# Kernel optimization log

Measured on AMD Instinct MI355X. Metric: run time of the kernel, lower is better.

The kernel has to match this reference:

```python
import jax, jax.numpy as jnp
import numpy as np

DIM, DEPTH, HEADS, DIM_HEAD, MLP_DIM = 512, 6, 8, 64, 2048
INNER = HEADS * DIM_HEAD
EPS = 1e-5


def _layernorm(x, s, b):
    mu = jnp.mean(x, axis=-1, keepdims=True)
    var = jnp.mean(jnp.square(x - mu), axis=-1, keepdims=True)
    return (x - mu) * jax.lax.rsqrt(var + EPS) * s + b


def setup_inputs() -> dict:
    key = jax.random.key(0)
    ks = jax.random.split(key, 12)
    d = {
        "x": jax.random.normal(ks[0], (8, 1024, DIM), dtype=jnp.float32),
        "ln1_s": jnp.ones((DEPTH, DIM), jnp.float32),
        "ln1_b": jnp.zeros((DEPTH, DIM), jnp.float32),
        "w_qkv": jax.random.normal(ks[1], (DEPTH, DIM, 3 * INNER), dtype=jnp.float32) * (DIM ** -0.5),
        "w_out": jax.random.normal(ks[2], (DEPTH, INNER, DIM), dtype=jnp.float32) * (INNER ** -0.5),
        "b_out": jnp.zeros((DEPTH, DIM), jnp.float32),
        "ln2_s": jnp.ones((DEPTH, DIM), jnp.float32),
        "ln2_b": jnp.zeros((DEPTH, DIM), jnp.float32),
        "w1": jax.random.normal(ks[3], (DEPTH, DIM, MLP_DIM), dtype=jnp.float32) * (DIM ** -0.5),
        "b1": jnp.zeros((DEPTH, MLP_DIM), jnp.float32),
        "w2": jax.random.normal(ks[4], (DEPTH, MLP_DIM, DIM), dtype=jnp.float32) * (MLP_DIM ** -0.5),
        "b2": jnp.zeros((DEPTH, DIM), jnp.float32),
    }
    return d


def reference(x, ln1_s, ln1_b, w_qkv, w_out, b_out, ln2_s, ln2_b, w1, b1, w2, b2):
    b, n, _ = x.shape
    scale = DIM_HEAD ** -0.5
    for i in range(DEPTH):
        # --- PreNorm Attention with residual ---
        h = _layernorm(x, ln1_s[i], ln1_b[i])
        qkv = h @ w_qkv[i]                                  # [b, n, 3*inner]
        q, k, v = jnp.split(qkv, 3, axis=-1)
        q = q.reshape(b, n, HEADS, DIM_HEAD)
        k = k.reshape(b, n, HEADS, DIM_HEAD)
        v = v.reshape(b, n, HEADS, DIM_HEAD)
        dots = jnp.einsum('bihd,bjhd->bhij', q, k) * scale  # [b, h, n, n]
        attn = jax.nn.softmax(dots, axis=-1)
        out = jnp.einsum('bhij,bjhd->bihd', attn, v).reshape(b, n, INNER)
        x = out @ w_out[i] + b_out[i] + x
        # --- PreNorm FeedForward with residual ---
        h = _layernorm(x, ln2_s[i], ln2_b[i])
        h = jax.nn.gelu(h @ w1[i] + b1[i], approximate=False)
        x = h @ w2[i] + b2[i] + x
    return x
```

## Files before the change

kernel.cpp:

```cpp
#include <hip/hip_runtime.h>
#include <cstdint>
#include <cstddef>

#define M_TOK 8192
#define DIMM  512
#define HEADS 8
#define DH    64
#define MLPD  2048
#define DEPTH 6

typedef unsigned short u16;
typedef unsigned int   u32;
typedef __attribute__((ext_vector_type(8))) short short8;
typedef __attribute__((ext_vector_type(4))) float f32x4;

__device__ __forceinline__ float bf2f(u16 u){ return __uint_as_float(((u32)u) << 16); }
__device__ __forceinline__ u16 f2bf(float f){
    u32 x = __float_as_uint(f);
    u32 r = x + 0x7fffu + ((x >> 16) & 1u);
    return (u16)(r >> 16);
}
__device__ __forceinline__ u32 cvt_pk_bf16(float a, float b){
    u32 r;
    asm("v_cvt_pk_bf16_f32 %0, %1, %2" : "=v"(r) : "v"(a), "v"(b));
    return r;
}
__device__ __forceinline__ void async16(const u16* g, u16* l){
    __builtin_amdgcn_global_load_lds(
        (const __attribute__((address_space(1))) void*)(uintptr_t)(const void*)g,
        (__attribute__((address_space(3))) void*)(u32)(uintptr_t)(void*)l,
        16, 0, 0);
}

__global__ void k_transpose_cvt(const float* __restrict__ in, u16* __restrict__ out, int R, int C){
    __shared__ u16 tile[32][33];
    size_t zoff = (size_t)blockIdx.z * R * C;
    in += zoff; out += zoff;
    int c0 = blockIdx.x * 32, r0 = blockIdx.y * 32;
    int tx = threadIdx.x, ty = threadIdx.y;
    #pragma unroll
    for (int i = 0; i < 32; i += 8)
        tile[ty + i][tx] = f2bf(in[(size_t)(r0 + ty + i) * C + c0 + tx]);
    __syncthreads();
    #pragma unroll
    for (int i = 0; i < 32; i += 8)
        out[(size_t)(c0 + ty + i) * R + r0 + tx] = tile[tx][ty + i];
}

__global__ __launch_bounds__(256) void k_layernorm(const float* __restrict__ x,
                                                   const float* __restrict__ s,
                                                   const float* __restrict__ b,
                                                   u16* __restrict__ out){
    int row = blockIdx.x * 4 + (threadIdx.x >> 6);
    int lane = threadIdx.x & 63;
    const float* xp = x + (size_t)row * DIMM + lane * 8;
    float v[8];
    #pragma unroll
    for (int c = 0; c < 8; c++) v[c] = xp[c];
    float sum = 0.f, sq = 0.f;
    #pragma unroll
    for (int c = 0; c < 8; c++){ sum += v[c]; sq += v[c] * v[c]; }
    #pragma unroll
    for (int m = 32; m >= 1; m >>= 1){
        sum += __shfl_xor(sum, m);
        sq  += __shfl_xor(sq,  m);
    }
    float mu  = sum * (1.f / DIMM);
    float var = sq * (1.f / DIMM) - mu * mu;
    float rs  = rsqrtf(var + 1e-5f);
    u16* op = out + (size_t)row * DIMM + lane * 8;
    #pragma unroll
    for (int c = 0; c < 8; c++){
        int col = lane * 8 + c;
        op[c] = f2bf((v[c] - mu) * rs * s[col] + b[col]);
    }
}

__device__ __forceinline__ float gelu_exact(float v){
    return 0.5f * v * (1.f + erff(v * 0.70710678118654752f));
}

#define LDT64 72

template<int MODE>
__global__ __launch_bounds__(256) void k_gemm128b(const u16* __restrict__ A,
                                                  const u16* __restrict__ Bt,
                                                  const float* __restrict__ bias,
                                                  u16* __restrict__ Cout,
                                                  int M, int N, int K){
    __shared__ u16 As[128 * LDT64];
    __shared__ u16 Bs[128 * LDT64];
    int m0 = blockIdx.y * 128, n0 = blockIdx.x * 128;
    int t = threadIdx.x;
    int w = t >> 6, lane = t & 63;
    int mi = lane & 15, quad = lane >> 4;
    int wr = w >> 1, wc = w & 1;

    int grow = lane >> 3, gcol = (lane & 7) * 8;
    const u16* agl = A  + (size_t)(m0 + w * 32 + grow) * K + gcol;
    const u16* bgl = Bt + (size_t)(n0 + w * 32 + grow) * K + gcol;
    u16* asl = &As[(w * 32) * 64];
    u16* bsl = &Bs[(w * 32) * 64];

    f32x4 acc[4][4];
    #pragma unroll
    for (int mt = 0; mt < 4; mt++)
        #pragma unroll
        for (int nt = 0; nt < 4; nt++) acc[mt][nt] = (f32x4){0.f, 0.f, 0.f, 0.f};

    for (int k0 = 0; k0 < K; k0 += 64){
        __syncthreads();
        #pragma unroll
        for (int i = 0; i < 4; i++){
            async16(agl + (size_t)(i * 8) * K + k0, asl + i * 8 * 64);
            async16(bgl + (size_t)(i * 8) * K + k0, bsl + i * 8 * 64);
        }
        __syncthreads();
        #pragma unroll
        for (int kk = 0; kk < 64; kk += 32){
            short8 af[4], bf[4];
            #pragma unroll
            for (int mt = 0; mt < 4; mt++)
                af[mt] = *(const short8*)&As[(wr * 64 + mt * 16 + mi) * 64 + kk + quad * 8];
            #pragma unroll
            for (int nt = 0; nt < 4; nt++)
                bf[nt] = *(const short8*)&Bs[(wc * 64 + nt * 16 + mi) * 64 + kk + quad * 8];
            #pragma unroll
            for (int mt = 0; mt < 4; mt++)
                #pragma unroll
                for (int nt = 0; nt < 4; nt++)
                    acc[mt][nt] = __builtin_amdgcn_mfma_f32_16x16x32_bf16(af[mt], bf[nt], acc[mt][nt], 0, 0, 0);
        }
    }

    float bv[4];
    if (MODE == 1){
        #pragma unroll
        for (int nt = 0; nt < 4; nt++) bv[nt] = bias[n0 + wc * 64 + nt * 16 + mi];
    }
    __syncthreads();
    u16* cs = &As[w * 16 * LDT64];
    int erow = lane >> 2, ecol = (lane & 3) * 16;
    #pragma unroll
    for (int mt = 0; mt < 4; mt++){
        #pragma unroll
        for (int nt = 0; nt < 4; nt++)
            #pragma unroll
            for (int r = 0; r < 4; r++){
                float v = acc[mt][nt][r];
                if (MODE == 1) v = gelu_exact(v + bv[nt]);
                cs[(quad * 4 + r) * LDT64 + nt * 16 + mi] = f2bf(v);
            }
        uint4 c0 = *(const uint4*)&cs[erow * LDT64 + ecol];
        uint4 c1 = *(const uint4*)&cs[erow * LDT64 + ecol + 8];
        u16* cp = Cout + (size_t)(m0 + wr * 64 + mt * 16 + erow) * N + n0 + wc * 64 + ecol;
        *(uint4*)cp       = c0;
        *(uint4*)(cp + 8) = c1;
    }
}

__global__ __launch_bounds__(256) void k_gemm64_res(const u16* __restrict__ A,
                                                    const u16* __restrict__ Bt,
                                                    const float* __restrict__ bias,
                                                    float* __restrict__ xres,
                                                    int M, int N, int K){
    __shared__ u16 As[64 * LDT64];
    __shared__ u16 Bs[64 * LDT64];
    int m0 = blockIdx.y * 64, n0 = blockIdx.x * 64;
    int t = threadIdx.x;
    int w = t >> 6, lane = t & 63;
    int mi = lane & 15, quad = lane >> 4;

    int grow = lane >> 3, gcol = (lane & 7) * 8;
    const u16* agl = A  + (size_t)(m0 + w * 16 + grow) * K + gcol;
    const u16* bgl = Bt + (size_t)(n0 + w * 16 + grow) * K + gcol;
    u16* asl = &As[(w * 16) * 64];
    u16* bsl = &Bs[(w * 16) * 64];

    f32x4 acc[4];
    #pragma unroll
    for (int tt = 0; tt < 4; tt++) acc[tt] = (f32x4){0.f, 0.f, 0.f, 0.f};

    for (int k0 = 0; k0 < K; k0 += 64){
        __syncthreads();
        #pragma unroll
        for (int i = 0; i < 2; i++){
            async16(agl + (size_t)(i * 8) * K + k0, asl + i * 8 * 64);
            async16(bgl + (size_t)(i * 8) * K + k0, bsl + i * 8 * 64);
        }
        __syncthreads();
        short8 af0 = *(const short8*)&As[(w * 16 + mi) * 64 + quad * 8];
        short8 af1 = *(const short8*)&As[(w * 16 + mi) * 64 + quad * 8 + 32];
        #pragma unroll
        for (int tt = 0; tt < 4; tt++){
            short8 bf0 = *(const short8*)&Bs[(tt * 16 + mi) * 64 + quad * 8];
            short8 bf1 = *(const short8*)&Bs[(tt * 16 + mi) * 64 + quad * 8 + 32];
            acc[tt] = __builtin_amdgcn_mfma_f32_16x16x32_bf16(af0, bf0, acc[tt], 0, 0, 0);
            acc[tt] = __builtin_amdgcn_mfma_f32_16x16x32_bf16(af1, bf1, acc[tt], 0, 0, 0);
        }
    }

    float bv[4];
    #pragma unroll
    for (int tt = 0; tt < 4; tt++) bv[tt] = bias[n0 + tt * 16 + mi];
    __syncthreads();
    float* cs = (w < 2) ? ((float*)As + w * 16 * LDT64)
                        : ((float*)Bs + (w - 2) * 16 * LDT64);
    #pragma unroll
    for (int tt = 0; tt < 4; tt++)
        #pragma unroll
        for (int r = 0; r < 4; r++)
            cs[(quad * 4 + r) * LDT64 + tt * 16 + mi] = acc[tt][r] + bv[tt];
    int erow = lane >> 2, ecol = (lane & 3) * 16;
    float* xp = xres + (size_t)(m0 + w * 16 + erow) * N + n0 + ecol;
    #pragma unroll
    for (int j = 0; j < 4; j++){
        float4 cv = *(const float4*)&cs[erow * LDT64 + ecol + j * 4];
        float4 xv = *(const float4*)(xp + j * 4);
        xv.x += cv.x; xv.y += cv.y; xv.z += cv.z; xv.w += cv.w;
        *(float4*)(xp + j * 4) = xv;
    }
}

#define LDK 72
#define C1_LOG2E 0.18033688011112042f
#define C2_LOG2E 11.541560327111707f

__global__ __launch_bounds__(256) void k_flash(const u16* __restrict__ qkv, u16* __restrict__ out){
    __shared__ u16 Ks[64 * LDK];
    __shared__ u16 Vt[80 * LDK];
    __shared__ u16 Ps[4][32 * LDK];
    int wg = (blockIdx.x & 7) * 64 + (blockIdx.x >> 3);
    int qt = wg & 7, h = (wg >> 3) & 7, b = wg >> 6;
    int t = threadIdx.x;
    int w = t >> 6, lane = t & 63;
    int mi = lane & 15, quad = lane >> 4;

    for (int i = t; i < 16 * 64; i += 256){
        int d = i >> 6, kk = i & 63;
        Vt[(64 + d) * LDK + kk] = 0x3F80;
    }

    const u16* base = qkv + ((size_t)b * 1024) * 1536;
    int hoff = h * 64;

    short8 qf[2][2];
    #pragma unroll
    for (int qh = 0; qh < 2; qh++){
        int qrow = qt * 128 + w * 32 + qh * 16 + mi;
        const u16* qp = base + (size_t)qrow * 1536 + hoff + quad * 8;
        qf[qh][0] = *(const short8*)(qp);
        qf[qh][1] = *(const short8*)(qp + 32);
    }

    f32x4 o[2][4];
    f32x4 lacc[2];
    #pragma unroll
    for (int qh = 0; qh < 2; qh++){
        #pragma unroll
        for (int nb = 0; nb < 4; nb++) o[qh][nb] = (f32x4){0.f, 0.f, 0.f, 0.f};
        lacc[qh] = (f32x4){0.f, 0.f, 0.f, 0.f};
    }

    int kkey = t >> 2, kseg = t & 3;
    const u16* kgp = base + (size_t)kkey * 1536 + 512 + hoff + kseg * 16;
    int vkey = lane, vdg = w;
    const u16* vgp = base + (size_t)vkey * 1536 + 1024 + hoff + vdg * 16;

    for (int kt = 0; kt < 16; kt++){
        size_t koff = (size_t)kt * 64 * 1536;
        uint4 kv0 = *(const uint4*)(kgp + koff);
        uint4 kv1 = *(const uint4*)(kgp + koff + 8);
        uint4 vv0 = *(const uint4*)(vgp + koff);
        uint4 vv1 = *(const uint4*)(vgp + koff + 8);
        __syncthreads();
        *(uint4*)&Ks[kkey * LDK + kseg * 16]     = kv0;
        *(uint4*)&Ks[kkey * LDK + kseg * 16 + 8] = kv1;
        u16 vtmp[16];
        *(uint4*)&vtmp[0] = vv0;
        *(uint4*)&vtmp[8] = vv1;
        #pragma unroll
        for (int i = 0; i < 16; i++)
            Vt[(vdg * 16 + i) * LDK + vkey] = vtmp[i];
        __syncthreads();

        short8 kb[4][2];
        #pragma unroll
        for (int nb = 0; nb < 4; nb++){
            kb[nb][0] = *(const short8*)&Ks[(nb * 16 + mi) * LDK + quad * 8];
            kb[nb][1] = *(const short8*)&Ks[(nb * 16 + mi) * LDK + quad * 8 + 32];
        }
        #pragma unroll
        for (int qh = 0; qh < 2; qh++){
            #pragma unroll
            for (int nb = 0; nb < 4; nb++){
                f32x4 z = (f32x4){0.f, 0.f, 0.f, 0.f};
                z = __builtin_amdgcn_mfma_f32_16x16x32_bf16(qf[qh][0], kb[nb][0], z, 0, 0, 0);
                z = __builtin_amdgcn_mfma_f32_16x16x32_bf16(qf[qh][1], kb[nb][1], z, 0, 0, 0);
                float e0 = exp2f(fmaf(z[0], C1_LOG2E, -C2_LOG2E));
                float e1 = exp2f(fmaf(z[1], C1_LOG2E, -C2_LOG2E));
                float e2 = exp2f(fmaf(z[2], C1_LOG2E, -C2_LOG2E));
                float e3 = exp2f(fmaf(z[3], C1_LOG2E, -C2_LOG2E));
                u32 p01 = cvt_pk_bf16(e0, e1);
                u32 p23 = cvt_pk_bf16(e2, e3);
                u16* pp = &Ps[w][(qh * 16 + quad * 4) * LDK + nb * 16 + mi];
                pp[0]       = (u16)p01;
                pp[LDK]     = (u16)(p01 >> 16);
                pp[2 * LDK] = (u16)p23;
                pp[3 * LDK] = (u16)(p23 >> 16);
            }
        }
        short8 vb[4][2], lb[2];
        #pragma unroll
        for (int nb = 0; nb < 4; nb++){
            vb[nb][0] = *(const short8*)&Vt[(nb * 16 + mi) * LDK + quad * 8];
            vb[nb][1] = *(const short8*)&Vt[(nb * 16 + mi) * LDK + quad * 8 + 32];
        }
        lb[0] = *(const short8*)&Vt[(64 + mi) * LDK + quad * 8];
        lb[1] = *(const short8*)&Vt[(64 + mi) * LDK + quad * 8 + 32];
        #pragma unroll
        for (int qh = 0; qh < 2; qh++){
            const short8 a0 = *(const short8*)&Ps[w][(qh * 16 + mi) * LDK + quad * 8];
            const short8 a1 = *(const short8*)&Ps[w][(qh * 16 + mi) * LDK + quad * 8 + 32];
            #pragma unroll
            for (int nb = 0; nb < 4; nb++){
                o[qh][nb] = __builtin_amdgcn_mfma_f32_16x16x32_bf16(a0, vb[nb][0], o[qh][nb], 0, 0, 0);
                o[qh][nb] = __builtin_amdgcn_mfma_f32_16x16x32_bf16(a1, vb[nb][1], o[qh][nb], 0, 0, 0);
            }
            lacc[qh] = __builtin_amdgcn_mfma_f32_16x16x32_bf16(a0, lb[0], lacc[qh], 0, 0, 0);
            lacc[qh] = __builtin_amdgcn_mfma_f32_16x16x32_bf16(a1, lb[1], lacc[qh], 0, 0, 0);
        }
    }
    #pragma unroll
    for (int qh = 0; qh < 2; qh++){
        float invl[4];
        #pragma unroll
        for (int r = 0; r < 4; r++) invl[r] = 1.f / lacc[qh][r];
        u16* op = out + ((size_t)b * 1024 + qt * 128 + w * 32 + qh * 16) * 512 + hoff;
        #pragma unroll
        for (int nb = 0; nb < 4; nb++){
            u32 c01 = cvt_pk_bf16(o[qh][nb][0] * invl[0], o[qh][nb][1] * invl[1]);
            u32 c23 = cvt_pk_bf16(o[qh][nb][2] * invl[2], o[qh][nb][3] * invl[3]);
            u16* cp = op + (size_t)(quad * 4) * 512 + nb * 16 + mi;
            cp[0]       = (u16)c01;
            cp[512]     = (u16)(c01 >> 16);
            cp[2 * 512] = (u16)c23;
            cp[3 * 512] = (u16)(c23 >> 16);
        }
    }
}

extern "C" void kernel_launch(void* const* d_in, const int* in_sizes, int n_in,
                              void* d_out, int out_size, void* d_ws, size_t ws_size,
                              hipStream_t stream){
    const float* x_in  = (const float*)d_in[0];
    const float* ln1_s = (const float*)d_in[1];
    const float* ln1_b = (const float*)d_in[2];
    const float* w_qkv = (const float*)d_in[3];
    const float* w_out = (const float*)d_in[4];
    const float* b_out = (const float*)d_in[5];
    const float* ln2_s = (const float*)d_in[6];
    const float* ln2_b = (const float*)d_in[7];
    const float* w1    = (const float*)d_in[8];
    const float* b1    = (const float*)d_in[9];
    const float* w2    = (const float*)d_in[10];
    const float* b2    = (const float*)d_in[11];
    float* out = (float*)d_out;

    char* ws = (char*)d_ws;
    float* x_f32 = (float*)ws;   ws += (size_t)M_TOK * DIMM * 4;
    u16* bufA    = (u16*)ws;     ws += (size_t)M_TOK * DIMM * 2;
    u16* bufB    = (u16*)ws;     ws += (size_t)M_TOK * MLPD * 2;
    u16* wbase   = (u16*)ws;
    size_t per_layer_w = (size_t)(1536 + 512 + 2048 + 2048) * 512;

    size_t used_big = (size_t)(ws - (char*)d_ws) + per_layer_w * 2 * DEPTH;
    bool big = (ws_size >= used_big);

    u16* ln_out   = bufA;
    u16* attn_out = bufA;
    u16* qkv      = bufB;
    u16* mlp_h    = bufB;

    size_t x_bytes = (size_t)M_TOK * DIMM * sizeof(float);
    hipMemcpyAsync(x_f32, x_in, x_bytes, hipMemcpyDeviceToDevice, stream);

    const size_t off_qkv = 0;
    const size_t off_out = (size_t)1536 * 512;
    const size_t off_w1  = off_out + (size_t)512 * 512;
    const size_t off_w2  = off_w1 + (size_t)2048 * 512;

    if (big){
        k_transpose_cvt<<<dim3(48, 16, 6), dim3(32, 8), 0, stream>>>(w_qkv, wbase + off_qkv * DEPTH, 512, 1536);
        k_transpose_cvt<<<dim3(16, 16, 6), dim3(32, 8), 0, stream>>>(w_out, wbase + off_out * DEPTH, 512, 512);
        k_transpose_cvt<<<dim3(64, 16, 6), dim3(32, 8), 0, stream>>>(w1,    wbase + off_w1  * DEPTH, 512, 2048);
        k_transpose_cvt<<<dim3(16, 64, 6), dim3(32, 8), 0, stream>>>(w2,    wbase + off_w2  * DEPTH, 2048, 512);
    }

    for (int i = 0; i < DEPTH; i++){
        u16 *wqkvT, *woutT, *w1T, *w2T;
        if (big){
            wqkvT = wbase + off_qkv * DEPTH + (size_t)i * 1536 * 512;
            woutT = wbase + off_out * DEPTH + (size_t)i * 512 * 512;
            w1T   = wbase + off_w1  * DEPTH + (size_t)i * 2048 * 512;
            w2T   = wbase + off_w2  * DEPTH + (size_t)i * 512 * 2048;
        } else {
            wqkvT = wbase + off_qkv; woutT = wbase + off_out;
            w1T   = wbase + off_w1;  w2T   = wbase + off_w2;
            k_transpose_cvt<<<dim3(48, 16), dim3(32, 8), 0, stream>>>(w_qkv + (size_t)i * 512 * 1536, wqkvT, 512, 1536);
            k_transpose_cvt<<<dim3(16, 16), dim3(32, 8), 0, stream>>>(w_out + (size_t)i * 512 * 512,  woutT, 512, 512);
            k_transpose_cvt<<<dim3(64, 16), dim3(32, 8), 0, stream>>>(w1    + (size_t)i * 512 * 2048, w1T,   512, 2048);
            k_transpose_cvt<<<dim3(16, 64), dim3(32, 8), 0, stream>>>(w2    + (size_t)i * 2048 * 512, w2T,   2048, 512);
        }

        k_layernorm<<<dim3(M_TOK / 4), dim3(256), 0, stream>>>(x_f32, ln1_s + i * 512, ln1_b + i * 512, ln_out);
        k_gemm128b<0><<<dim3(12, 64), dim3(256), 0, stream>>>(ln_out, wqkvT, nullptr, qkv,
                                                              M_TOK, 1536, 512);
        k_flash<<<dim3(512), dim3(256), 0, stream>>>(qkv, attn_out);
        k_gemm64_res<<<dim3(8, 128), dim3(256), 0, stream>>>(attn_out, woutT, b_out + i * 512, x_f32,
                                                             M_TOK, 512, 512);
        k_layernorm<<<dim3(M_TOK / 4), dim3(256), 0, stream>>>(x_f32, ln2_s + i * 512, ln2_b + i * 512, ln_out);
        k_gemm128b<1><<<dim3(16, 64), dim3(256), 0, stream>>>(ln_out, w1T, b1 + i * 2048, mlp_h,
                                                              M_TOK, 2048, 512);
        k_gemm64_res<<<dim3(8, 128), dim3(256), 0, stream>>>(mlp_h, w2T, b2 + i * 512, x_f32,
                                                             M_TOK, 512, 2048);
    }
    hipMemcpyAsync(out, x_f32, x_bytes, hipMemcpyDeviceToDevice, stream);
}
```

Before: 1.332 ms.

## Double-buffer GEMM shared tiles and prefetch next K/V tile in attention

Both GEMM kernels now keep two shared-memory tile buffers and issue the async global-to-LDS loads for the next K slice while MFMAs run on the current one. This drops one barrier per iteration and hides global load latency. The attention kernel also loads the next K/V tile into registers right after the current tile is staged in LDS, so that load overlaps the QK and PV math. In exchange, LDS use per block doubles, which may lower occupancy. The epilogue reuses the As buffer with a padded stride over the now unpadded arrays, which happens to fit.

Result: faster. 1.263 ms (-5.2%).

```diff
diff --git a/kernel.cpp b/kernel.cpp
--- a/kernel.cpp
+++ b/kernel.cpp
@@ -88,8 +88,8 @@
                                                   const float* __restrict__ bias,
                                                   u16* __restrict__ Cout,
                                                   int M, int N, int K){
-    __shared__ u16 As[128 * LDT64];
-    __shared__ u16 Bs[128 * LDT64];
+    __shared__ u16 As[2][128 * 64];
+    __shared__ u16 Bs[2][128 * 64];
     int m0 = blockIdx.y * 128, n0 = blockIdx.x * 128;
     int t = threadIdx.x;
     int w = t >> 6, lane = t & 63;
@@ -99,8 +99,6 @@
     int grow = lane >> 3, gcol = (lane & 7) * 8;
     const u16* agl = A  + (size_t)(m0 + w * 32 + grow) * K + gcol;
     const u16* bgl = Bt + (size_t)(n0 + w * 32 + grow) * K + gcol;
-    u16* asl = &As[(w * 32) * 64];
-    u16* bsl = &Bs[(w * 32) * 64];
 
     f32x4 acc[4][4];
     #pragma unroll
@@ -108,29 +106,48 @@
         #pragma unroll
         for (int nt = 0; nt < 4; nt++) acc[mt][nt] = (f32x4){0.f, 0.f, 0.f, 0.f};
 
-    for (int k0 = 0; k0 < K; k0 += 64){
-        __syncthreads();
+    int nt_k = K >> 6;
+    {
+        u16* asl = &As[0][(w * 32) * 64];
+        u16* bsl = &Bs[0][(w * 32) * 64];
         #pragma unroll
         for (int i = 0; i < 4; i++){
-            async16(agl + (size_t)(i * 8) * K + k0, asl + i * 8 * 64);
-            async16(bgl + (size_t)(i * 8) * K + k0, bsl + i * 8 * 64);
-        }
-        __syncthreads();
+            async16(agl + (size_t)(i * 8) * K, asl + i * 8 * 64);
+            async16(bgl + (size_t)(i * 8) * K, bsl + i * 8 * 64);
+        }
+    }
+    __syncthreads();
+
+    for (int td = 0; td < nt_k; td++){
+        int cur = td & 1;
+        if (td + 1 < nt_k){
+            int k0 = (td + 1) << 6;
+            u16* asl = &As[cur ^ 1][(w * 32) * 64];
+            u16* bsl = &Bs[cur ^ 1][(w * 32) * 64];
+            #pragma unroll
+            for (int i = 0; i < 4; i++){
+                async16(agl + (size_t)(i * 8) * K + k0, asl + i * 8 * 64);
+                async16(bgl + (size_t)(i * 8) * K + k0, bsl + i * 8 * 64);
+            }
+        }
+        const u16* Ab = &As[cur][0];
+        const u16* Bb = &Bs[cur][0];
         #pragma unroll
         for (int kk = 0; kk < 64; kk += 32){
             short8 af[4], bf[4];
             #pragma unroll
             for (int mt = 0; mt < 4; mt++)
-                af[mt] = *(const short8*)&As[(wr * 64 + mt * 16 + mi) * 64 + kk + quad * 8];
+                af[mt] = *(const short8*)&Ab[(wr * 64 + mt * 16 + mi) * 64 + kk + quad * 8];
             #pragma unroll
             for (int nt = 0; nt < 4; nt++)
-                bf[nt] = *(const short8*)&Bs[(wc * 64 + nt * 16 + mi) * 64 + kk + quad * 8];
+                bf[nt] = *(const short8*)&Bb[(wc * 64 + nt * 16 + mi) * 64 + kk + quad * 8];
             #pragma unroll
             for (int mt = 0; mt < 4; mt++)
                 #pragma unroll
                 for (int nt = 0; nt < 4; nt++)
                     acc[mt][nt] = __builtin_amdgcn_mfma_f32_16x16x32_bf16(af[mt], bf[nt], acc[mt][nt], 0, 0, 0);
         }
+        __syncthreads();
     }
 
     float bv[4];
@@ -138,8 +155,7 @@
         #pragma unroll
         for (int nt = 0; nt < 4; nt++) bv[nt] = bias[n0 + wc * 64 + nt * 16 + mi];
     }
-    __syncthreads();
-    u16* cs = &As[w * 16 * LDT64];
+    u16* cs = ((u16*)As) + w * 16 * LDT64;
     int erow = lane >> 2, ecol = (lane & 3) * 16;
     #pragma unroll
     for (int mt = 0; mt < 4; mt++){
@@ -164,8 +180,8 @@
                                                     const float* __restrict__ bias,
                                                     float* __restrict__ xres,
                                                     int M, int N, int K){
-    __shared__ u16 As[64 * LDT64];
-    __shared__ u16 Bs[64 * LDT64];
+    __shared__ u16 As[2][64 * 64];
+    __shared__ u16 Bs[2][64 * 64];
     int m0 = blockIdx.y * 64, n0 = blockIdx.x * 64;
     int t = threadIdx.x;
     int w = t >> 6, lane = t & 63;
@@ -174,36 +190,52 @@
     int grow = lane >> 3, gcol = (lane & 7) * 8;
     const u16* agl = A  + (size_t)(m0 + w * 16 + grow) * K + gcol;
     const u16* bgl = Bt + (size_t)(n0 + w * 16 + grow) * K + gcol;
-    u16* asl = &As[(w * 16) * 64];
-    u16* bsl = &Bs[(w * 16) * 64];
 
     f32x4 acc[4];
     #pragma unroll
     for (int tt = 0; tt < 4; tt++) acc[tt] = (f32x4){0.f, 0.f, 0.f, 0.f};
 
-    for (int k0 = 0; k0 < K; k0 += 64){
-        __syncthreads();
+    int nt_k = K >> 6;
+    {
+        u16* asl = &As[0][(w * 16) * 64];
+        u16* bsl = &Bs[0][(w * 16) * 64];
         #pragma unroll
         for (int i = 0; i < 2; i++){
-            async16(agl + (size_t)(i * 8) * K + k0, asl + i * 8 * 64);
-            async16(bgl + (size_t)(i * 8) * K + k0, bsl + i * 8 * 64);
-        }
-        __syncthreads();
-        short8 af0 = *(const short8*)&As[(w * 16 + mi) * 64 + quad * 8];
-        short8 af1 = *(const short8*)&As[(w * 16 + mi) * 64 + quad * 8 + 32];
+            async16(agl + (size_t)(i * 8) * K, asl + i * 8 * 64);
+            async16(bgl + (size_t)(i * 8) * K, bsl + i * 8 * 64);
+        }
+    }
+    __syncthreads();
+
+    for (int td = 0; td < nt_k; td++){
+        int cur = td & 1;
+        if (td + 1 < nt_k){
+            int k0 = (td + 1) << 6;
+            u16* asl = &As[cur ^ 1][(w * 16) * 64];
+            u16* bsl = &Bs[cur ^ 1][(w * 16) * 64];
+            #pragma unroll
+            for (int i = 0; i < 2; i++){
+                async16(agl + (size_t)(i * 8) * K + k0, asl + i * 8 * 64);
+                async16(bgl + (size_t)(i * 8) * K + k0, bsl + i * 8 * 64);
+            }
+        }
+        const u16* Ab = &As[cur][0];
+        const u16* Bb = &Bs[cur][0];
+        short8 af0 = *(const short8*)&Ab[(w * 16 + mi) * 64 + quad * 8];
+        short8 af1 = *(const short8*)&Ab[(w * 16 + mi) * 64 + quad * 8 + 32];
         #pragma unroll
         for (int tt = 0; tt < 4; tt++){
-            short8 bf0 = *(const short8*)&Bs[(tt * 16 + mi) * 64 + quad * 8];
-            short8 bf1 = *(const short8*)&Bs[(tt * 16 + mi) * 64 + quad * 8 + 32];
+            short8 bf0 = *(const short8*)&Bb[(tt * 16 + mi) * 64 + quad * 8];
+            short8 bf1 = *(const short8*)&Bb[(tt * 16 + mi) * 64 + quad * 8 + 32];
             acc[tt] = __builtin_amdgcn_mfma_f32_16x16x32_bf16(af0, bf0, acc[tt], 0, 0, 0);
             acc[tt] = __builtin_amdgcn_mfma_f32_16x16x32_bf16(af1, bf1, acc[tt], 0, 0, 0);
         }
+        __syncthreads();
     }
 
     float bv[4];
     #pragma unroll
     for (int tt = 0; tt < 4; tt++) bv[tt] = bias[n0 + tt * 16 + mi];
-    __syncthreads();
     float* cs = (w < 2) ? ((float*)As + w * 16 * LDT64)
                         : ((float*)Bs + (w - 2) * 16 * LDT64);
     #pragma unroll
@@ -267,12 +299,12 @@
     int vkey = lane, vdg = w;
     const u16* vgp = base + (size_t)vkey * 1536 + 1024 + hoff + vdg * 16;
 
+    uint4 kv0 = *(const uint4*)(kgp);
+    uint4 kv1 = *(const uint4*)(kgp + 8);
+    uint4 vv0 = *(const uint4*)(vgp);
+    uint4 vv1 = *(const uint4*)(vgp + 8);
+
     for (int kt = 0; kt < 16; kt++){
-        size_t koff = (size_t)kt * 64 * 1536;
-        uint4 kv0 = *(const uint4*)(kgp + koff);
-        uint4 kv1 = *(const uint4*)(kgp + koff + 8);
-        uint4 vv0 = *(const uint4*)(vgp + koff);
-        uint4 vv1 = *(const uint4*)(vgp + koff + 8);
         __syncthreads();
         *(uint4*)&Ks[kkey * LDK + kseg * 16]     = kv0;
         *(uint4*)&Ks[kkey * LDK + kseg * 16 + 8] = kv1;
@@ -283,6 +315,14 @@
         for (int i = 0; i < 16; i++)
             Vt[(vdg * 16 + i) * LDK + vkey] = vtmp[i];
         __syncthreads();
+
+        if (kt < 15){
+            size_t koff = (size_t)(kt + 1) * 64 * 1536;
+            kv0 = *(const uint4*)(kgp + koff);
+            kv1 = *(const uint4*)(kgp + koff + 8);
+            vv0 = *(const uint4*)(vgp + koff);
+            vv1 = *(const uint4*)(vgp + koff + 8);
+        }
 
         short8 kb[4][2];
         #pragma unroll
```
